# Optimization experiments

Measured on AMD Instinct MI355X. Metric: run time of the kernel, lower is better.

The kernel has to match this reference:

```python
import jax, jax.numpy as jnp
import numpy as np

B, N, S, K = 32, 2048, 64, 128   # clouds, pts/cloud, fps centers (ratio=64/2048), max neighbors
R = 0.2                          # radius ball-query
SLOPE = 0.2                      # LeakyReLU negative slope
C_CONV = [3, 64, 128, 512]       # PointConv local nn
D_FEAT = 512


def leaky(x):
    return jnp.where(x >= 0, x, SLOPE * x)


def _init_linear(key, din, dout):
    kw, kb = jax.random.split(key)
    lim = 1.0 / np.sqrt(din)
    W = jax.random.uniform(kw, (din, dout), minval=-lim, maxval=lim, dtype=jnp.float32)
    b = jax.random.uniform(kb, (dout,), minval=-lim, maxval=lim, dtype=jnp.float32)
    return W, b


def setup_inputs() -> dict:
    key = jax.random.key(0)
    ks = jax.random.split(key, 6)
    pos = jax.random.uniform(ks[0], (B * N, 3), dtype=jnp.float32)
    batch = (jnp.arange(B * N, dtype=jnp.int32) // N)
    W1, b1 = _init_linear(ks[1], 3, 64)
    W2, b2 = _init_linear(ks[2], 64, 128)
    W3, b3 = _init_linear(ks[3], 128, 512)
    W4, b4 = _init_linear(ks[4], D_FEAT + 3, 512)
    W5, b5 = _init_linear(ks[5], 512, 1024)
    return {"pos": pos, "batch": batch,
            "W1": W1, "b1": b1, "W2": W2, "b2": b2, "W3": W3, "b3": b3,
            "W4": W4, "b4": b4, "W5": W5, "b5": b5}


def _fps_one(p):
    """Deterministic farthest point sampling on one cloud p:[N,3] -> idx:[S]."""
    d0 = jnp.sum((p - p[0]) ** 2, axis=-1)

    def step(dists, _):
        nxt = jnp.argmax(dists).astype(jnp.int32)
        dists = jnp.minimum(dists, jnp.sum((p - p[nxt]) ** 2, axis=-1))
        return dists, nxt

    _, rest = jax.lax.scan(step, d0, None, length=S - 1)
    return jnp.concatenate([jnp.zeros((1,), jnp.int32), rest])


def _encoder(pos, W1, b1, W2, b2, W3, b3, W4, b4, W5, b5):
    pts = pos.reshape(B, N, 3)
    idx = jax.vmap(_fps_one)(pts)                                   # [B,S] local fps indices
    centers = jnp.take_along_axis(pts, idx[:, :, None], axis=1)     # [B,S,3]

    # radius ball query (first-by-index up to K neighbors, like torch_cluster cap)
    d2 = jnp.sum((centers[:, :, None, :] - pts[:, None, :, :]) ** 2, axis=-1)  # [B,S,N]
    inball = d2 < R * R
    keys = jnp.where(inball, jnp.arange(N, dtype=jnp.int32)[None, None, :], N)
    nbr = jnp.sort(keys, axis=-1)[:, :, :K]                          # [B,S,K]
    valid = nbr < N
    nbr = jnp.where(valid, nbr, 0)

    # PointConv: gather relative positions -> MLP -> masked max aggregation
    nbr_pos = jnp.take_along_axis(pts[:, None, :, :], nbr[..., None], axis=2)  # [B,S,K,3]
    rel = nbr_pos - centers[:, :, None, :]
    h = leaky(rel @ W1 + b1)
    h = leaky(h @ W2 + b2)
    h = leaky(h @ W3 + b3)                                           # [B,S,K,512]
    h = jnp.where(valid[..., None], h, -jnp.inf)
    feat = jnp.max(h, axis=2)                                        # [B,S,512] (self always in ball)

    g = jnp.concatenate([feat, centers], axis=-1).reshape(B * S, D_FEAT + 3)
    g = leaky(g @ W4 + b4)
    out = g @ W5 + b5                                                # [B*S,1024]
    mean, logvar = out[:, :512], out[:, 512:]
    std = jnp.exp(0.5 * logvar)

    # global edge indices (x_idx = neighbor point id, y_idx = center id), -1 padded
    x_idx = jnp.where(valid, nbr + jnp.arange(B, dtype=jnp.int32)[:, None, None] * N, -1).reshape(-1)
    y_idx = jnp.where(valid, jnp.arange(B * S, dtype=jnp.int32).reshape(B, S, 1), -1).reshape(-1)
    return mean, std, x_idx, y_idx


def reference(pos, batch, W1, b1, W2, b2, W3, b3, W4, b4, W5, b5):
    # batch is implied by the fixed [B,N] layout (sorted, equal-size clouds)
    return _encoder(pos, W1, b1, W2, b2, W3, b3, W4, b4, W5, b5)
```

## Files before the change

kernel.cpp:

```cpp
#include <hip/hip_runtime.h>
#include <hip/hip_bf16.h>

#define NB 32
#define NP 2048
#define NS 64
#define NK 128

#define MEAN_OFF 0
#define STD_OFF  1048576
#define XIDX_OFF 2097152
#define YIDX_OFF 2359296

#define GA_LD 576

typedef __attribute__((ext_vector_type(4)))  short s4;
typedef __attribute__((ext_vector_type(8)))  short short8;
typedef __attribute__((ext_vector_type(16))) float f32x16;

static __device__ __forceinline__ float leaky(float x){ return x >= 0.0f ? x : 0.2f * x; }

static __device__ __forceinline__ unsigned short bf16u(float v){
    __hip_bfloat16 h = __float2bfloat16(v);
    return *(unsigned short*)&h;
}

static __device__ __forceinline__ unsigned cvtpk(float a, float b){
    unsigned d;
    asm("v_cvt_pk_bf16_f32 %0, %1, %2" : "=v"(d) : "v"(a), "v"(b));
    return d;
}
static __device__ __forceinline__ void plswap(unsigned &a, unsigned &b){
    asm volatile("v_permlane32_swap_b32 %0, %1" : "+v"(a), "+v"(b));
}

static __device__ __forceinline__ float d2s(float ax,float ay,float az,float bx,float by,float bz){
    float dx = __fsub_rn(ax,bx), dy = __fsub_rn(ay,by), dz = __fsub_rn(az,bz);
    return __fadd_rn(__fadd_rn(__fmul_rn(dx,dx),__fmul_rn(dy,dy)),__fmul_rn(dz,dz));
}

__global__ __launch_bounds__(256) void fps_prep_kernel(const float* __restrict__ pos,
                                                       float* __restrict__ centersWs,
                                                       const float* __restrict__ W2,
                                                       const float* __restrict__ W3,
                                                       const float* __restrict__ W4,
                                                       const float* __restrict__ W5,
                                                       __hip_bfloat16* __restrict__ W2T,
                                                       __hip_bfloat16* __restrict__ W3T,
                                                       __hip_bfloat16* __restrict__ W4T,
                                                       __hip_bfloat16* __restrict__ W5T)
{
    if (blockIdx.x >= NB) {
        __shared__ float tl[64][65];
        int tb = blockIdx.x - NB;
        int t = threadIdx.x;
        int tr = t >> 6;
        int tc = t & 63;
        if (tb < 72) {
            int kt = tb >> 3, nt = tb & 7;
            int k0 = kt*64, n0 = nt*64;
            #pragma unroll
            for (int it = 0; it < 16; it++) {
                int k = k0 + tr + it*4;
                tl[tr + it*4][tc] = (k < 515) ? W4[(size_t)k*512 + n0 + tc] : 0.0f;
            }
            __syncthreads();
            #pragma unroll
            for (int it = 0; it < 16; it++) {
                int nl = tr + it*4;
                W4T[(size_t)(n0 + nl)*GA_LD + k0 + tc] = __float2bfloat16(tl[tc][nl]);
            }
        } else if (tb < 200) {
            int q = tb - 72;
            int kt = q >> 4, nt = q & 15;
            int k0 = kt*64, n0 = nt*64;
            #pragma unroll
            for (int it = 0; it < 16; it++)
                tl[tr + it*4][tc] = W5[(size_t)(k0 + tr + it*4)*1024 + n0 + tc];
            __syncthreads();
            #pragma unroll
            for (int it = 0; it < 16; it++) {
                int nl = tr + it*4;
                W5T[(size_t)(n0 + nl)*512 + k0 + tc] = __float2bfloat16(tl[tc][nl]);
            }
        } else if (tb < 216) {
            int q = tb - 200;
            int i0 = (q >> 3)*64, c0 = (q & 7)*64;
            #pragma unroll
            for (int it = 0; it < 16; it++)
                tl[tr + it*4][tc] = W3[(size_t)(i0 + tr + it*4)*512 + c0 + tc];
            __syncthreads();
            #pragma unroll
            for (int it = 0; it < 16; it++) {
                int c = c0 + tr + it*4;
                int i = i0 + tc;
                int byte = c*256 + ((i*2) ^ ((c&15)<<4));
                *(unsigned short*)((char*)W3T + byte) = bf16u(tl[tc][tr + it*4]);
            }
        } else {
            for (int e = t; e < 8192; e += 256) {
                int i = e & 127, j = e >> 7;
                W2T[i*64 + j] = __float2bfloat16(W2[(size_t)j*128 + i]);
            }
        }
        return;
    }

    int b = blockIdx.x;
    int t = threadIdx.x;
    __shared__ float redv[2][4];
    __shared__ int   redi[2][4];
    __shared__ float cwr[2][4];
    __shared__ float cbuf[NS*3];

    const float* pb = pos + (size_t)b * NP * 3;
    float rx[8], ry[8], rz[8], dl[8];
    #pragma unroll
    for (int q = 0; q < 8; q++) {
        int n = t + q*256;
        rx[q] = pb[n*3+0]; ry[q] = pb[n*3+1]; rz[q] = pb[n*3+2];
    }

    float cx = pb[0], cy = pb[1], cz = pb[2];
    if (t == 0) { cbuf[0] = cx; cbuf[1] = cy; cbuf[2] = cz; }

    float bv = -1.0f; int bi = 0;
    #pragma unroll
    for (int q = 0; q < 8; q++) {
        dl[q] = d2s(rx[q],ry[q],rz[q], cx,cy,cz);
        if (dl[q] > bv) { bv = dl[q]; bi = t + q*256; }
    }

    int w = t >> 6;
    for (int s = 1; s < NS; s++) {
        #pragma unroll
        for (int m = 32; m > 0; m >>= 1) {
            float ov = __shfl_xor(bv, m);
            int   oi = __shfl_xor(bi, m);
            if (ov > bv || (ov == bv && oi < bi)) { bv = ov; bi = oi; }
        }
        int s1 = s & 1;
        if ((t & 63) == 0) { redv[s1][w] = bv; redi[s1][w] = bi; }
        __syncthreads();
        float v = redv[s1][0]; int j = redi[s1][0];
        #pragma unroll
        for (int k = 1; k < 4; k++) {
            if (redv[s1][k] > v || (redv[s1][k] == v && redi[s1][k] < j)) { v = redv[s1][k]; j = redi[s1][k]; }
        }
        if (t == (j & 255)) {
            int qq = j >> 8;
            float ox = rx[0], oy = ry[0], oz = rz[0];
            #pragma unroll
            for (int q = 1; q < 8; q++)
                if (q == qq) { ox = rx[q]; oy = ry[q]; oz = rz[q]; }
            cwr[s1][0] = ox; cwr[s1][1] = oy; cwr[s1][2] = oz;
            cbuf[s*3+0] = ox; cbuf[s*3+1] = oy; cbuf[s*3+2] = oz;
        }
        __syncthreads();
        cx = cwr[s1][0]; cy = cwr[s1][1]; cz = cwr[s1][2];
        bv = -1.0f; bi = 0;
        #pragma unroll
        for (int q = 0; q < 8; q++) {
            float nd = fminf(dl[q], d2s(rx[q],ry[q],rz[q], cx,cy,cz));
            dl[q] = nd;
            if (nd > bv) { bv = nd; bi = t + q*256; }
        }
    }
    __syncthreads();
    for (int e = t; e < NS*3; e += 256)
        centersWs[(size_t)b*NS*3 + e] = cbuf[e];
}

__global__ __launch_bounds__(256, 4) void ball_mlp_kernel(
    const float* __restrict__ pos,
    const float* __restrict__ W1, const float* __restrict__ b1,
    const float* __restrict__ b2, const float* __restrict__ b3,
    const __hip_bfloat16* __restrict__ W2Tp,
    const __hip_bfloat16* __restrict__ W3Tp,
    const float* __restrict__ centersWs,
    float* __restrict__ out,
    __hip_bfloat16* __restrict__ gAb)
{
    __shared__ char smem[37392];
    char*  h1s  = smem;
    float* relL = (float*)(smem + 32768);
    int*   nbL  = (int*)(smem + 32768);
    float* b2s  = (float*)(smem + 34816);
    float* b3s  = (float*)(smem + 35328);
    int*   cntW4= (int*)(smem + 37376);

    const short* W2T  = (const short*)W2Tp;
    const char*  W3Tb = (const char*)W3Tp;

    int r = blockIdx.x, b = r >> 6, tid = threadIdx.x;
    int l = tid & 63, w = tid >> 6;
    int l31 = l & 31;
    int hsel = l >> 5;
    int jsel8 = hsel * 8;
    int colsel = hsel * 16;

#define STAGE_W3(CH, DST)                                                                              \
    {                                                                                                  \
        const char* _s = W3Tb + (CH)*8192 + w*2048 + l*16;                                             \
        char* _d = (DST) + w*2048;                                                                     \
        __builtin_amdgcn_global_load_lds((const __attribute__((address_space(1))) void*)(_s),          \
                                         (__attribute__((address_space(3))) void*)(_d), 16, 0, 0);     \
        __builtin_amdgcn_global_load_lds((const __attribute__((address_space(1))) void*)(_s + 1024),   \
                                         (__attribute__((address_space(3))) void*)(_d + 1024), 16, 0, 0); \
    }

    STAGE_W3(0, smem + 16384);
    STAGE_W3(1, smem + 24576);

    float cx = centersWs[r*3+0], cy = centersWs[r*3+1], cz = centersWs[r*3+2];

    const float* pb = pos + (size_t)b * NP * 3;
    {
        int myCnt = 0;
        #pragma unroll
        for (int c = 0; c < 8; c++) {
            int n = w*512 + c*64 + l;
            float x = pb[n*3+0], y = pb[n*3+1], z = pb[n*3+2];
            bool in = d2s(cx,cy,cz, x,y,z) < 0.04f;
            unsigned long long m = __ballot(in);
            int before = __popcll(m & ((1ull << l) - 1ull));
            int p = myCnt + before;
            if (in && p < NK) nbL[w*NK + p] = n;
            myCnt += (int)__popcll(m);
        }
        if (l == 0) cntW4[w] = myCnt;
    }
    b3s[tid] = b3[tid];
    b3s[tid + 256] = b3[tid + 256];
    __syncthreads();

    int c0 = cntW4[0], c1 = cntW4[1], c2 = cntW4[2], c3 = cntW4[3];
    int cnt = c0 + c1 + c2 + c3;
    cnt = cnt > NK ? NK : cnt;

    int nv = 0;
    if (tid < NK) {
        bool valid = tid < cnt;
        int seg = 0, off = 0;
        if (tid >= c0)           { seg = 1; off = c0; }
        if (tid >= c0 + c1)      { seg = 2; off = c0 + c1; }
        if (tid >= c0 + c1 + c2) { seg = 3; off = c0 + c1 + c2; }
        if (valid) nv = nbL[seg*NK + (tid - off)];
        out[XIDX_OFF + r*NK + tid] = valid ? (float)(nv + b*NP) : -1.0f;
        out[YIDX_OFF + r*NK + tid] = valid ? (float)r : -1.0f;
    }
    __syncthreads();

    if (tid < NK) {
        const float* pp = pb + (size_t)nv*3;
        relL[tid*4+0] = pp[0] - cx;
        relL[tid*4+1] = pp[1] - cy;
        relL[tid*4+2] = pp[2] - cz;
        relL[tid*4+3] = 0.0f;
        b2s[tid] = b2[tid];
    }
    __syncthreads();

    {
        int jg = (tid & 15) * 4;
        float4 w0 = *(const float4*)&W1[jg];
        float4 w1 = *(const float4*)&W1[64 + jg];
        float4 w2 = *(const float4*)&W1[128 + jg];
        float4 bb = *(const float4*)&b1[jg];
        #pragma unroll
        for (int e = 0; e < 8; e++) {
            int k = (tid >> 4) + e*16;
            float4 r4 = *(const float4*)&relL[k*4];
            s4 pk;
            pk[0] = (short)bf16u(leaky(bb.x + r4.x*w0.x + r4.y*w1.x + r4.z*w2.x));
            pk[1] = (short)bf16u(leaky(bb.y + r4.x*w0.y + r4.y*w1.y + r4.z*w2.y));
            pk[2] = (short)bf16u(leaky(bb.z + r4.x*w0.z + r4.y*w1.z + r4.z*w2.z));
            pk[3] = (short)bf16u(leaky(bb.w + r4.x*w0.w + r4.y*w1.w + r4.z*w2.w));
            *(s4*)(h1s + k*128 + ((jg*2) ^ ((k&7)<<4))) = pk;
        }
    }
    __syncthreads();

    short8 a3[8];
    {
        int kcol = w*32 + l31;
        short8 bh[4];
        #pragma unroll
        for (int ks = 0; ks < 4; ks++) {
            int bc = ks*32 + colsel;
            bh[ks] = *(short8*)(h1s + kcol*128 + (bc ^ ((kcol&7)<<4)));
        }
        #pragma unroll
        for (int it = 0; it < 4; it++) {
            short8 aWf[4];
            #pragma unroll
            for (int ks = 0; ks < 4; ks++)
                aWf[ks] = *(const short8*)(W2T + (it*32 + l31)*64 + ks*16 + jsel8);
            f32x16 acc;
            #pragma unroll
            for (int q = 0; q < 16; q++) acc[q] = 0.f;
            #pragma unroll
            for (int ks = 0; ks < 4; ks++)
                acc = __builtin_amdgcn_mfma_f32_32x32x16_bf16(aWf[ks], bh[ks], acc, 0, 0, 0);
            int ibase = it*32 + 4*hsel;
            #pragma unroll
            for (int g = 0; g < 4; g++) {
                float4 bb = *(const float4*)&b2s[ibase + g*8];
                acc[g*4+0] = leaky(acc[g*4+0] + bb.x);
                acc[g*4+1] = leaky(acc[g*4+1] + bb.y);
                acc[g*4+2] = leaky(acc[g*4+2] + bb.z);
                acc[g*4+3] = leaky(acc[g*4+3] + bb.w);
            }
            #pragma unroll
            for (int hf = 0; hf < 2; hf++) {
                unsigned A0 = cvtpk(acc[hf*8+0], acc[hf*8+1]);
                unsigned A1 = cvtpk(acc[hf*8+2], acc[hf*8+3]);
                unsigned B0 = cvtpk(acc[hf*8+4], acc[hf*8+5]);
                unsigned B1 = cvtpk(acc[hf*8+6], acc[hf*8+7]);
                plswap(A0, B0);
                plswap(A1, B1);
                union { unsigned u[4]; short8 s; } f;
                f.u[0] = A0; f.u[1] = A1; f.u[2] = B0; f.u[3] = B1;
                a3[2*it + hf] = f.s;
            }
        }
    }
    __syncthreads();

    STAGE_W3(2, smem);
    STAGE_W3(3, smem + 8192);

    int kb0 = w*32 + 4*hsel;
    float mred[16];
    #pragma unroll
    for (int t = 0; t < 16; t++) {
        if (t <= 13)      { asm volatile("s_waitcnt vmcnt(4)" ::: "memory"); }
        else if (t == 14) { asm volatile("s_waitcnt vmcnt(2)" ::: "memory"); }
        else              { asm volatile("s_waitcnt vmcnt(0)" ::: "memory"); }
        __builtin_amdgcn_sched_barrier(0);
        __builtin_amdgcn_s_barrier();
        __builtin_amdgcn_sched_barrier(0);

        if (t >= 1 && t + 3 < 16) {
            char* nbuf = smem + 8192*((t+1)&3);
            STAGE_W3(t+3, nbuf);
        }
        __builtin_amdgcn_sched_barrier(0);

        char* buf = smem + 8192*((t+2)&3);
        f32x16 acc;
        #pragma unroll
        for (int q = 0; q < 16; q++) acc[q] = 0.f;
        #pragma unroll
        for (int ks = 0; ks < 8; ks++) {
            int bc = ks*32 + colsel;
            short8 bv = *(short8*)(buf + l31*256 + (bc ^ ((l31&15)<<4)));
            acc = __builtin_amdgcn_mfma_f32_32x32x16_bf16(a3[ks], bv, acc, 0, 0, 0);
        }
        float m = -INFINITY;
        #pragma unroll
        for (int reg = 0; reg < 16; reg++) {
            int kloc = (reg&3) + 8*(reg>>2);
            if (kb0 + kloc < cnt) m = fmaxf(m, acc[reg]);
        }
        m = fmaxf(m, __shfl_xor(m, 32));
        mred[t] = m;
        __builtin_amdgcn_sched_barrier(0);
    }

    float* redf = (float*)(smem + 16384);
    if (l < 32) {
        #pragma unroll
        for (int t = 0; t < 16; t++)
            redf[w*512 + t*32 + l31] = mred[t];
    }
    __syncthreads();
    #pragma unroll
    for (int e = 0; e < 2; e++) {
        int c = tid + e*256;
        float m = fmaxf(fmaxf(redf[c], redf[512 + c]), fmaxf(redf[1024 + c], redf[1536 + c]));
        gAb[(size_t)r*GA_LD + c] = __float2bfloat16(leaky(m + b3s[c]));
    }
    if (tid < 64) {
        float v = 0.0f;
        if (tid == 0) v = cx; else if (tid == 1) v = cy; else if (tid == 2) v = cz;
        gAb[(size_t)r*GA_LD + 512 + tid] = __float2bfloat16(v);
    }
#undef STAGE_W3
}

__global__ __launch_bounds__(256) void fc1_kernel(const __hip_bfloat16* __restrict__ gAb,
                                                  const __hip_bfloat16* __restrict__ W4T,
                                                  const float* __restrict__ b4,
                                                  __hip_bfloat16* __restrict__ g2b)
{
    __shared__ char smem[16384];
    char* As = smem;
    char* Bs = smem + 8192;

    int bx = blockIdx.x & 7;
    int by = blockIdx.x >> 3;
    int tid = threadIdx.x;
    int l = tid & 63, w = tid >> 6;
    int wm = w & 1, wn = w >> 1;
    int colsel = (l >> 5) * 16;

    f32x16 acc;
    #pragma unroll
    for (int q = 0; q < 16; q++) acc[q] = 0.f;

    int ra = wm*32 + (l & 31);
    int rn = wn*32 + (l & 31);

    for (int kb = 0; kb < GA_LD; kb += 64) {
        #pragma unroll
        for (int it = 0; it < 2; it++) {
            int e = it*256 + tid;
            int row = e >> 3, seg = e & 7;
            short8 va = *(const short8*)(gAb + (size_t)(by*64 + row)*GA_LD + kb + seg*8);
            *(short8*)(As + row*128 + ((seg*16) ^ ((row&7)<<4))) = va;
            short8 vb = *(const short8*)(W4T + (size_t)(bx*64 + row)*GA_LD + kb + seg*8);
            *(short8*)(Bs + row*128 + ((seg*16) ^ ((row&7)<<4))) = vb;
        }
        __syncthreads();
        #pragma unroll
        for (int ks = 0; ks < 4; ks++) {
            int bc = ks*32 + colsel;
            short8 av = *(short8*)(As + ra*128 + (bc ^ ((ra&7)<<4)));
            short8 bv = *(short8*)(Bs + rn*128 + (bc ^ ((rn&7)<<4)));
            acc = __builtin_amdgcn_mfma_f32_32x32x16_bf16(av, bv, acc, 0, 0, 0);
        }
        __syncthreads();
    }

    int col = bx*64 + wn*32 + (l & 31);
    float bcol = b4[col];
    int rbase = by*64 + wm*32 + 4*(l>>5);
    #pragma unroll
    for (int reg = 0; reg < 16; reg++) {
        int row = rbase + (reg&3) + 8*(reg>>2);
        g2b[(size_t)row*512 + col] = __float2bfloat16(leaky(acc[reg] + bcol));
    }
}

__global__ __launch_bounds__(256) void fc2_kernel(const __hip_bfloat16* __restrict__ g2b,
                                                  const __hip_bfloat16* __restrict__ W5T,
                                                  const float* __restrict__ b5,
                                                  float* __restrict__ out)
{
    __shared__ char smem[16384];
    char* As = smem;
    char* Bs = smem + 8192;

    int bx = blockIdx.x & 15;
    int by = blockIdx.x >> 4;
    int tid = threadIdx.x;
    int l = tid & 63, w = tid >> 6;
    int wm = w & 1, wn = w >> 1;
    int colsel = (l >> 5) * 16;

    f32x16 acc;
    #pragma unroll
    for (int q = 0; q < 16; q++) acc[q] = 0.f;

    int ra = wm*32 + (l & 31);
    int rn = wn*32 + (l & 31);

    for (int kb = 0; kb < 512; kb += 64) {
        #pragma unroll
        for (int it = 0; it < 2; it++) {
            int e = it*256 + tid;
            int row = e >> 3, seg = e & 7;
            short8 va = *(const short8*)(g2b + (size_t)(by*64 + row)*512 + kb + seg*8);
            *(short8*)(As + row*128 + ((seg*16) ^ ((row&7)<<4))) = va;
            short8 vb = *(const short8*)(W5T + (size_t)(bx*64 + row)*512 + kb + seg*8);
            *(short8*)(Bs + row*128 + ((seg*16) ^ ((row&7)<<4))) = vb;
        }
        __syncthreads();
        #pragma unroll
        for (int ks = 0; ks < 4; ks++) {
            int bc = ks*32 + colsel;
            short8 av = *(short8*)(As + ra*128 + (bc ^ ((ra&7)<<4)));
            short8 bv = *(short8*)(Bs + rn*128 + (bc ^ ((rn&7)<<4)));
            acc = __builtin_amdgcn_mfma_f32_32x32x16_bf16(av, bv, acc, 0, 0, 0);
        }
        __syncthreads();
    }

    int col = bx*64 + wn*32 + (l & 31);
    float bcol = b5[col];
    int rbase = by*64 + wm*32 + 4*(l>>5);
    #pragma unroll
    for (int reg = 0; reg < 16; reg++) {
        int row = rbase + (reg&3) + 8*(reg>>2);
        float v = acc[reg] + bcol;
        if (col < 512) {
            out[MEAN_OFF + (size_t)row*512 + col] = v;
        } else {
            out[STD_OFF + (size_t)row*512 + (col - 512)] = expf(0.5f*v);
        }
    }
}

extern "C" void kernel_launch(void* const* d_in, const int* in_sizes, int n_in,
                              void* d_out, int out_size, void* d_ws, size_t ws_size,
                              hipStream_t stream) {
    const float* pos = (const float*)d_in[0];
    const float* W1  = (const float*)d_in[2];
    const float* b1  = (const float*)d_in[3];
    const float* W2  = (const float*)d_in[4];
    const float* b2  = (const float*)d_in[5];
    const float* W3  = (const float*)d_in[6];
    const float* b3  = (const float*)d_in[7];
    const float* W4  = (const float*)d_in[8];
    const float* b4  = (const float*)d_in[9];
    const float* W5  = (const float*)d_in[10];
    const float* b5  = (const float*)d_in[11];
    float* out = (float*)d_out;

    char* ws = (char*)d_ws;
    float* centersWs = (float*)(ws);
    __hip_bfloat16* gAb = (__hip_bfloat16*)(ws + 1081344);
    __hip_bfloat16* g2b = (__hip_bfloat16*)(ws + 3440640);
    __hip_bfloat16* W2T = (__hip_bfloat16*)(ws + 5537792);
    __hip_bfloat16* W3T = (__hip_bfloat16*)(ws + 5554176);
    __hip_bfloat16* W4T = (__hip_bfloat16*)(ws + 5685248);
    __hip_bfloat16* W5T = (__hip_bfloat16*)(ws + 6275072);

    hipLaunchKernelGGL(fps_prep_kernel, dim3(NB + 217), dim3(256), 0, stream,
                       pos, centersWs, W2, W3, W4, W5, W2T, W3T, W4T, W5T);
    hipLaunchKernelGGL(ball_mlp_kernel, dim3(NB*NS), dim3(256), 0, stream,
                       pos, W1,b1, b2,b3, W2T, W3T, centersWs, out, gAb);
    hipLaunchKernelGGL(fc1_kernel, dim3(256), dim3(256), 0, stream, gAb, W4T, b4, g2b);
    hipLaunchKernelGGL(fc2_kernel, dim3(512), dim3(256), 0, stream, g2b, W5T, b5, out);
}
```

Before: 146.5 us.

## Run FPS on a single wavefront with DPP reductions and LDS point lookup

Farthest point sampling now runs on a single 64-lane wavefront per cloud instead of four. Each lane holds 32 points, so the per-step block barriers and LDS cross-wave reduction go away. The argmax reduction uses DPP row shifts for the first stages and shuffles for the rest, and the selected center is read from an LDS copy of the cloud. The trade-off is 4x more serial distance work per lane, more registers, and idle threads in the 256-thread block.

Measured after the change: 143.2 us. 2.2% less time.

```diff
diff --git a/kernel.cpp b/kernel.cpp
--- a/kernel.cpp
+++ b/kernel.cpp
@@ -31,6 +31,14 @@
 }
 static __device__ __forceinline__ void plswap(unsigned &a, unsigned &b){
     asm volatile("v_permlane32_swap_b32 %0, %1" : "+v"(a), "+v"(b));
+}
+
+template<int CTRL>
+static __device__ __forceinline__ void dpp_step(float &bv, int &bi){
+    int ovi = __builtin_amdgcn_update_dpp(0, __float_as_int(bv), CTRL, 0xF, 0xF, true);
+    int oi  = __builtin_amdgcn_update_dpp(0, bi, CTRL, 0xF, 0xF, true);
+    float ov = __int_as_float(ovi);
+    if (ov > bv || (ov == bv && oi < bi)) { bv = ov; bi = oi; }
 }
 
 static __device__ __forceinline__ float d2s(float ax,float ay,float az,float bx,float by,float bz){
@@ -105,19 +113,21 @@
         return;
     }
 
+    __shared__ float pxL[NP], pyL[NP], pzL[NP];
+    __shared__ float cbuf[NS*3];
+
+    int t = threadIdx.x;
+    if (t >= 64) return;
     int b = blockIdx.x;
-    int t = threadIdx.x;
-    __shared__ float redv[2][4];
-    __shared__ int   redi[2][4];
-    __shared__ float cwr[2][4];
-    __shared__ float cbuf[NS*3];
 
     const float* pb = pos + (size_t)b * NP * 3;
-    float rx[8], ry[8], rz[8], dl[8];
-    #pragma unroll
-    for (int q = 0; q < 8; q++) {
-        int n = t + q*256;
-        rx[q] = pb[n*3+0]; ry[q] = pb[n*3+1]; rz[q] = pb[n*3+2];
+    float rx[32], ry[32], rz[32], dl[32];
+    #pragma unroll
+    for (int q = 0; q < 32; q++) {
+        int n = t + q*64;
+        float x = pb[n*3+0], y = pb[n*3+1], z = pb[n*3+2];
+        rx[q] = x; ry[q] = y; rz[q] = z;
+        pxL[n] = x; pyL[n] = y; pzL[n] = z;
     }
 
     float cx = pb[0], cy = pb[1], cz = pb[2];
@@ -125,49 +135,40 @@
 
     float bv = -1.0f; int bi = 0;
     #pragma unroll
-    for (int q = 0; q < 8; q++) {
+    for (int q = 0; q < 32; q++) {
         dl[q] = d2s(rx[q],ry[q],rz[q], cx,cy,cz);
-        if (dl[q] > bv) { bv = dl[q]; bi = t + q*256; }
-    }
-
-    int w = t >> 6;
+        if (dl[q] > bv) { bv = dl[q]; bi = t + q*64; }
+    }
+
     for (int s = 1; s < NS; s++) {
-        #pragma unroll
-        for (int m = 32; m > 0; m >>= 1) {
-            float ov = __shfl_xor(bv, m);
-            int   oi = __shfl_xor(bi, m);
+        dpp_step<0x121>(bv, bi);
+        dpp_step<0x122>(bv, bi);
+        dpp_step<0x124>(bv, bi);
+        dpp_step<0x128>(bv, bi);
+        {
+            float ov = __shfl_xor(bv, 16);
+            int   oi = __shfl_xor(bi, 16);
             if (ov > bv || (ov == bv && oi < bi)) { bv = ov; bi = oi; }
         }
-        int s1 = s & 1;
-        if ((t & 63) == 0) { redv[s1][w] = bv; redi[s1][w] = bi; }
-        __syncthreads();
-        float v = redv[s1][0]; int j = redi[s1][0];
-        #pragma unroll
-        for (int k = 1; k < 4; k++) {
-            if (redv[s1][k] > v || (redv[s1][k] == v && redi[s1][k] < j)) { v = redv[s1][k]; j = redi[s1][k]; }
-        }
-        if (t == (j & 255)) {
-            int qq = j >> 8;
-            float ox = rx[0], oy = ry[0], oz = rz[0];
-            #pragma unroll
-            for (int q = 1; q < 8; q++)
-                if (q == qq) { ox = rx[q]; oy = ry[q]; oz = rz[q]; }
-            cwr[s1][0] = ox; cwr[s1][1] = oy; cwr[s1][2] = oz;
-            cbuf[s*3+0] = ox; cbuf[s*3+1] = oy; cbuf[s*3+2] = oz;
-        }
-        __syncthreads();
-        cx = cwr[s1][0]; cy = cwr[s1][1]; cz = cwr[s1][2];
+        {
+            float ov = __shfl_xor(bv, 32);
+            int   oi = __shfl_xor(bi, 32);
+            if (ov > bv || (ov == bv && oi < bi)) { bv = ov; bi = oi; }
+        }
+        int j = bi;
+        cx = pxL[j]; cy = pyL[j]; cz = pzL[j];
+        if (t == 0) { cbuf[s*3+0] = cx; cbuf[s*3+1] = cy; cbuf[s*3+2] = cz; }
         bv = -1.0f; bi = 0;
         #pragma unroll
-        for (int q = 0; q < 8; q++) {
+        for (int q = 0; q < 32; q++) {
             float nd = fminf(dl[q], d2s(rx[q],ry[q],rz[q], cx,cy,cz));
             dl[q] = nd;
-            if (nd > bv) { bv = nd; bi = t + q*256; }
-        }
-    }
-    __syncthreads();
-    for (int e = t; e < NS*3; e += 256)
-        centersWs[(size_t)b*NS*3 + e] = cbuf[e];
+            if (nd > bv) { bv = nd; bi = t + q*64; }
+        }
+    }
+    #pragma unroll
+    for (int e = 0; e < 3; e++)
+        centersWs[(size_t)b*NS*3 + t + e*64] = cbuf[t + e*64];
 }
 
 __global__ __launch_bounds__(256, 4) void ball_mlp_kernel(
```
